# Performance work log

Hardware: AMD Instinct MI355X
Metric: run time of the kernel (lower is better)

## Reference

```python
import jax, jax.numpy as jnp
import numpy as np

EPS = 1e-4  # Moller-Trumbore epsilon from the original

def _dot(a, b):
    return jnp.sum(a * b, axis=-1)

def setup_inputs() -> dict:
    key = jax.random.key(0)
    k1, k2, k3 = jax.random.split(key, 3)
    N, V, F = 2048, 2500, 4096
    p = jax.random.normal(k1, (N, 3), dtype=jnp.float32)
    v = jax.random.normal(k2, (V, 3), dtype=jnp.float32)
    f = jax.random.randint(k3, (F, 3), 0, V, dtype=jnp.int64)
    return {"p": p, "v": v, "f": f}

def reference(p, v, f):
    N = p.shape[0]
    faces = v[f]                      # (F,3,3)
    a, b, c = faces[:, 0], faces[:, 1], faces[:, 2]   # (F,3) each
    pe = p[None]                      # (1,N,3), broadcasts against (F,1,3)

    # --- point-to-triangle distance = min over the 3 edge segments (matches original output math) ---
    e1 = a - b                        # faces[:,0]-faces[:,1]
    e2 = c - b
    e3 = c - a

    def seg(e, ref_pt, q0, q1):
        # s = ((ref_pt - p) . e) / |e|^2, clamped; closest = s*q0 + (1-s)*q1  (original formula kept verbatim)
        m2 = _dot(e, e)[:, None]                       # (F,1)
        s = jnp.clip(_dot(ref_pt[:, None] - pe, e[:, None]) / m2, 0.0, 1.0)[..., None]  # (F,N,1)
        cl = s * q0[:, None] + (1.0 - s) * q1[:, None]  # (F,N,3)
        d = jnp.linalg.norm(cl - pe, axis=-1)           # (F,N)
        return d, cl

    d12, c12 = seg(e1, a, b, a)   # s12 from (p0-p).e1; closest = s*p1+(1-s)*p0
    d23, c23 = seg(e2, c, b, c)   # s23 from (p2-p).e2; closest = s*p1+(1-s)*p2
    d31, c31 = seg(e3, c, a, c)   # s31 from (p2-p).e3; closest = s*p0+(1-s)*p2

    d_all = jnp.stack([d12, d23, d31], axis=0)          # (3,F,N)
    c_all = jnp.stack([c12, c23, c31], axis=0)          # (3,F,N,3)
    which = jnp.argmin(d_all, axis=0)                   # (F,N)
    dist = jnp.min(d_all, axis=0)                       # (F,N)
    closest = jnp.take_along_axis(c_all, which[None, ..., None], axis=0)[0]  # (F,N,3)

    # nearest face per query point
    fidx = jnp.argmin(jnp.abs(dist), axis=0)            # (N,)
    dmin = jnp.take_along_axis(dist, fidx[None], axis=0)  # (1,N)
    closest_p = closest[fidx, jnp.arange(N)]            # (N,3)

    # --- Moller-Trumbore ray-triangle parity test toward mesh centroid ---
    dirv = v.mean(axis=0)[None] - p                     # (N,3)
    me1 = b - a                                         # faces[:,1]-faces[:,0]
    me2 = c - a
    pvec = jnp.cross(dirv[None], me2[:, None])          # (F,N,3)
    det = _dot(me1[:, None], pvec)                      # (F,N)
    tvec = pe - a[:, None]                              # (F,N,3)
    u = _dot(tvec, pvec) / det
    qvec = jnp.cross(tvec, me1[:, None])                # (F,N,3)
    dd = _dot(dirv[None], qvec) / det
    t = _dot(me2[:, None], qvec) / det
    hit = (jnp.abs(det) > EPS) & (u >= 0) & (u <= 1) & (dd >= 0) & (u + dd <= 1) & (t > EPS)
    counts = jnp.sum(hit, axis=0)                       # (N,)
    inside = (0.5 - (counts % 2 == 1).astype(dmin.dtype)) * 2.0  # +1 outside, -1 inside

    dmin = dmin * inside[None]                          # (1,N)
    return (dmin, closest_p)
```

## Files before the change

kernel.cpp:

```cpp
#include <hip/hip_runtime.h>
#include <math.h>

#define TRI_EPS 1e-4f

__global__ __launch_bounds__(256) void prep_kernel(
    const float* __restrict__ v, const int* __restrict__ f,
    float4* __restrict__ fdat, float* __restrict__ vm,
    unsigned long long* __restrict__ keys, int* __restrict__ hcnt,
    int V, int F, int N) {
    const int t = threadIdx.x;
    const int j = blockIdx.x * 256 + t;
    if (j < N) {
        keys[j] = 0xFFFFFFFFFFFFFFFFull;
        hcnt[j] = 0;
    }
    if (j < F) {
        const int i0 = f[3 * j + 0];
        const int i1 = f[3 * j + 1];
        const int i2 = f[3 * j + 2];
        const float ax = v[3 * i0 + 0], ay = v[3 * i0 + 1], az = v[3 * i0 + 2];
        const float bx = v[3 * i1 + 0], by = v[3 * i1 + 1], bz = v[3 * i1 + 2];
        const float cx = v[3 * i2 + 0], cy = v[3 * i2 + 1], cz = v[3 * i2 + 2];
        const float e1x = ax - bx, e1y = ay - by, e1z = az - bz;
        const float e2x = cx - bx, e2y = cy - by, e2z = cz - bz;
        const float e3x = cx - ax, e3y = cy - ay, e3z = cz - az;
        const float m1 = e1x * e1x + e1y * e1y + e1z * e1z;
        const float m2 = e2x * e2x + e2y * e2y + e2z * e2z;
        const float m3 = e3x * e3x + e3y * e3y + e3z * e3z;
        fdat[6 * j + 0] = make_float4(ax, ay, az, 1.f / m1);
        fdat[6 * j + 1] = make_float4(bx, by, bz, 1.f / m2);
        fdat[6 * j + 2] = make_float4(cx, cy, cz, 1.f / m3);
        fdat[6 * j + 3] = make_float4(e1x, e1y, e1z, 0.f);
        fdat[6 * j + 4] = make_float4(e2x, e2y, e2z, 0.f);
        fdat[6 * j + 5] = make_float4(e3x, e3y, e3z, 0.f);
    }
    if (blockIdx.x == 0) {
        __shared__ float sx[256], sy[256], sz[256];
        float x = 0.f, y = 0.f, z = 0.f;
        for (int i = t; i < V; i += 256) {
            x += v[3 * i + 0];
            y += v[3 * i + 1];
            z += v[3 * i + 2];
        }
        sx[t] = x; sy[t] = y; sz[t] = z;
        __syncthreads();
        for (int off = 128; off > 0; off >>= 1) {
            if (t < off) {
                sx[t] += sx[t + off];
                sy[t] += sy[t + off];
                sz[t] += sz[t + off];
            }
            __syncthreads();
        }
        if (t == 0) {
            vm[0] = sx[0] / (float)V;
            vm[1] = sy[0] / (float)V;
            vm[2] = sz[0] / (float)V;
        }
    }
}

struct FP {
    float d1, d2, d3;
    float x1, y1, z1, x2, y2, z2, x3, y3, z3;
    float apx, apy, apz;
};

__device__ __forceinline__ FP face_point(
    const float4 ra, const float4 rb, const float4 rc,
    const float e1x, const float e1y, const float e1z,
    const float e2x, const float e2y, const float e2z,
    const float e3x, const float e3y, const float e3z,
    const float px, const float py, const float pz) {
    FP r;
    const float ax = ra.x, ay = ra.y, az = ra.z;
    const float bx = rb.x, by = rb.y, bz = rb.z;
    const float cx = rc.x, cy = rc.y, cz = rc.z;
    r.apx = ax - px; r.apy = ay - py; r.apz = az - pz;
    const float cpx = cx - px, cpy = cy - py, cpz = cz - pz;

    float s1 = (r.apx * e1x + r.apy * e1y + r.apz * e1z) * ra.w;
    s1 = fminf(fmaxf(s1, 0.f), 1.f);
    const float o1 = 1.f - s1;
    r.x1 = s1 * bx + o1 * ax;
    r.y1 = s1 * by + o1 * ay;
    r.z1 = s1 * bz + o1 * az;
    float ux = r.x1 - px, uy = r.y1 - py, uz = r.z1 - pz;
    r.d1 = ux * ux + uy * uy + uz * uz;

    float s2 = (cpx * e2x + cpy * e2y + cpz * e2z) * rb.w;
    s2 = fminf(fmaxf(s2, 0.f), 1.f);
    const float o2 = 1.f - s2;
    r.x2 = s2 * bx + o2 * cx;
    r.y2 = s2 * by + o2 * cy;
    r.z2 = s2 * bz + o2 * cz;
    ux = r.x2 - px; uy = r.y2 - py; uz = r.z2 - pz;
    r.d2 = ux * ux + uy * uy + uz * uz;

    float s3 = (cpx * e3x + cpy * e3y + cpz * e3z) * rc.w;
    s3 = fminf(fmaxf(s3, 0.f), 1.f);
    const float o3 = 1.f - s3;
    r.x3 = s3 * ax + o3 * cx;
    r.y3 = s3 * ay + o3 * cy;
    r.z3 = s3 * az + o3 * cz;
    ux = r.x3 - px; uy = r.y3 - py; uz = r.z3 - pz;
    r.d3 = ux * ux + uy * uy + uz * uz;
    return r;
}

__device__ __forceinline__ void pair_update(
    const float4 ra, const float4 rb, const float4 rc,
    const float e1x, const float e1y, const float e1z,
    const float e2x, const float e2y, const float e2z,
    const float e3x, const float e3y, const float e3z,
    const float px, const float py, const float pz,
    const float dx, const float dy, const float dz, const int j,
    float& bd2, int& bid, int& hits) {
    const FP r = face_point(ra, rb, rc, e1x, e1y, e1z, e2x, e2y, e2z,
                            e3x, e3y, e3z, px, py, pz);
    float fd2 = r.d1; int eid = 0;
    if (r.d2 < fd2) { fd2 = r.d2; eid = 1; }
    if (r.d3 < fd2) { fd2 = r.d3; eid = 2; }
    if (fd2 < bd2) { bd2 = fd2; bid = (j << 2) | eid; }

    const float pvx = dy * e3z - dz * e3y;
    const float pvy = dz * e3x - dx * e3z;
    const float pvz = dx * e3y - dy * e3x;
    const float det = -(e1x * pvx + e1y * pvy + e1z * pvz);
    const float tu = -(r.apx * pvx + r.apy * pvy + r.apz * pvz);
    const float qvx = r.apy * e1z - r.apz * e1y;
    const float qvy = r.apz * e1x - r.apx * e1z;
    const float qvz = r.apx * e1y - r.apy * e1x;
    const float td = dx * qvx + dy * qvy + dz * qvz;
    const float tn = e3x * qvx + e3y * qvy + e3z * qvz;
    const float adet = fabsf(det);
    const float sd = (det > 0.f) ? 1.f : -1.f;
    const float su = tu * sd;
    const float sq = td * sd;
    const float st = tn * sd;
    if (adet > TRI_EPS && su >= 0.f && su <= adet && sq >= 0.f &&
        (su + sq) <= adet && st > TRI_EPS * adet)
        hits++;
}

__global__ __launch_bounds__(256) void sdf_main(
    const float* __restrict__ p, const float4* __restrict__ fd,
    const float* __restrict__ vm,
    unsigned long long* __restrict__ keys, int* __restrict__ hcnt,
    int N, int F, int C, int CS) {
    const int k = blockIdx.x % C;
    const int pg = blockIdx.x / C;
    const int i = pg * 256 + threadIdx.x;
    if (i >= N) return;

    const float px = p[3 * i + 0];
    const float py = p[3 * i + 1];
    const float pz = p[3 * i + 2];
    const float dx = vm[0] - px;
    const float dy = vm[1] - py;
    const float dz = vm[2] - pz;

    float bd2 = INFINITY;
    int bid = 0x7fffffff;
    int hits = 0;

    const int j0 = k * CS;
    const int j1 = min(F, j0 + CS);
    #pragma unroll 4
    for (int j = j0; j < j1; ++j) {
        const float4 ra  = fd[6 * j + 0];
        const float4 rb  = fd[6 * j + 1];
        const float4 rc  = fd[6 * j + 2];
        const float4 re1 = fd[6 * j + 3];
        const float4 re2 = fd[6 * j + 4];
        const float4 re3 = fd[6 * j + 5];
        pair_update(ra, rb, rc, re1.x, re1.y, re1.z, re2.x, re2.y, re2.z,
                    re3.x, re3.y, re3.z, px, py, pz, dx, dy, dz, j,
                    bd2, bid, hits);
    }
    const unsigned long long key =
        ((unsigned long long)__float_as_uint(bd2) << 32) | (unsigned int)bid;
    atomicMin(&keys[i], key);
    if (hits) atomicAdd(&hcnt[i], hits);
}

__global__ __launch_bounds__(256) void sdf_epilogue(
    const float* __restrict__ p, const float4* __restrict__ fd,
    const unsigned long long* __restrict__ keys, const int* __restrict__ hcnt,
    float* __restrict__ out, int N) {
    const int i = blockIdx.x * 256 + threadIdx.x;
    if (i >= N) return;
    const unsigned long long key = keys[i];
    const float bd2 = __uint_as_float((unsigned int)(key >> 32));
    const int bid = (int)(unsigned int)(key & 0xFFFFFFFFull);
    const int jw = bid >> 2;
    const int eid = bid & 3;
    const float px = p[3 * i + 0];
    const float py = p[3 * i + 1];
    const float pz = p[3 * i + 2];
    const float4 wa  = fd[6 * jw + 0];
    const float4 wb  = fd[6 * jw + 1];
    const float4 wc  = fd[6 * jw + 2];
    const float4 we1 = fd[6 * jw + 3];
    const float4 we2 = fd[6 * jw + 4];
    const float4 we3 = fd[6 * jw + 5];
    const FP r = face_point(wa, wb, wc, we1.x, we1.y, we1.z,
                            we2.x, we2.y, we2.z, we3.x, we3.y, we3.z,
                            px, py, pz);
    float clx = r.x1, cly = r.y1, clz = r.z1;
    if (eid == 1) { clx = r.x2; cly = r.y2; clz = r.z2; }
    if (eid == 2) { clx = r.x3; cly = r.y3; clz = r.z3; }
    const float d = sqrtf(bd2);
    out[i] = (hcnt[i] & 1) ? -d : d;
    out[N + 3 * i + 0] = clx;
    out[N + 3 * i + 1] = cly;
    out[N + 3 * i + 2] = clz;
}

extern "C" void kernel_launch(void* const* d_in, const int* in_sizes, int n_in,
                              void* d_out, int out_size, void* d_ws,
                              size_t ws_size, hipStream_t stream) {
    const float* p = (const float*)d_in[0];
    const float* v = (const float*)d_in[1];
    const int* f = (const int*)d_in[2];
    float* out = (float*)d_out;

    const int N = in_sizes[0] / 3;
    const int V = in_sizes[1] / 3;
    const int F = in_sizes[2] / 3;

    char* base = (char*)d_ws;
    float* vm = (float*)base;
    unsigned long long* keys = (unsigned long long*)(base + 16);
    int* hcnt = (int*)(base + 16 + 8ull * N);
    size_t off = 16 + 12ull * N;
    off = (off + 15) & ~15ull;
    float4* fdat = (float4*)(base + off);

    const int C = 256;
    const int CS = (F + C - 1) / C;
    const int npg = (N + 255) / 256;

    const int gprep = (max(F, N) + 255) / 256;
    prep_kernel<<<gprep, 256, 0, stream>>>(v, f, fdat, vm, keys, hcnt, V, F, N);
    sdf_main<<<npg * C, 256, 0, stream>>>(p, fdat, vm, keys, hcnt, N, F, C, CS);
    sdf_epilogue<<<(N + 255) / 256, 256, 0, stream>>>(p, fdat, keys, hcnt, out, N);
}
```

Baseline: 44.67 us.

## Stage face chunk in shared memory and process two points per thread

Adds a templated main kernel for the case F == 256*16 that loads each block's 16-face chunk (96 float4) into LDS once. Each thread then handles two query points, so every face record read is reused twice and the grid is halved. The intent is to cut global/L1 traffic for face data and to amortise the loads and atomics. In exchange each thread uses more registers, and the fast path is specialised to one exact face count, with a generic fallback kernel for other sizes.

```diff
diff --git a/kernel.cpp b/kernel.cpp
--- a/kernel.cpp
+++ b/kernel.cpp
@@ -143,7 +143,69 @@
         hits++;
 }
 
-__global__ __launch_bounds__(256) void sdf_main(
+template <int CS>
+__global__ __launch_bounds__(256) void sdf_main_t(
+    const float* __restrict__ p, const float4* __restrict__ fd,
+    const float* __restrict__ vm,
+    unsigned long long* __restrict__ keys, int* __restrict__ hcnt,
+    int N, int C) {
+    __shared__ float4 sfd[6 * CS];
+    const int t = threadIdx.x;
+    const int k = blockIdx.x % C;
+    const int pg = blockIdx.x / C;
+    const int j0 = k * CS;
+
+    if (t < 6 * CS) sfd[t] = fd[6 * j0 + t];
+
+    const int i0 = pg * 512 + t;
+    const int i1 = i0 + 256;
+    const bool vA = (i0 < N);
+    const bool vB = (i1 < N);
+    const int lA = vA ? i0 : 0;
+    const int lB = vB ? i1 : 0;
+    const float pAx = p[3 * lA + 0], pAy = p[3 * lA + 1], pAz = p[3 * lA + 2];
+    const float pBx = p[3 * lB + 0], pBy = p[3 * lB + 1], pBz = p[3 * lB + 2];
+    const float vmx = vm[0], vmy = vm[1], vmz = vm[2];
+    const float dAx = vmx - pAx, dAy = vmy - pAy, dAz = vmz - pAz;
+    const float dBx = vmx - pBx, dBy = vmy - pBy, dBz = vmz - pBz;
+
+    float Ad2 = INFINITY; int Aid = 0x7fffffff; int Ah = 0;
+    float Bd2 = INFINITY; int Bid = 0x7fffffff; int Bh = 0;
+
+    __syncthreads();
+
+    #pragma unroll 4
+    for (int jj = 0; jj < CS; ++jj) {
+        const float4 ra  = sfd[6 * jj + 0];
+        const float4 rb  = sfd[6 * jj + 1];
+        const float4 rc  = sfd[6 * jj + 2];
+        const float4 re1 = sfd[6 * jj + 3];
+        const float4 re2 = sfd[6 * jj + 4];
+        const float4 re3 = sfd[6 * jj + 5];
+        const int j = j0 + jj;
+        pair_update(ra, rb, rc, re1.x, re1.y, re1.z, re2.x, re2.y, re2.z,
+                    re3.x, re3.y, re3.z, pAx, pAy, pAz, dAx, dAy, dAz, j,
+                    Ad2, Aid, Ah);
+        pair_update(ra, rb, rc, re1.x, re1.y, re1.z, re2.x, re2.y, re2.z,
+                    re3.x, re3.y, re3.z, pBx, pBy, pBz, dBx, dBy, dBz, j,
+                    Bd2, Bid, Bh);
+    }
+
+    if (vA) {
+        const unsigned long long keyA =
+            ((unsigned long long)__float_as_uint(Ad2) << 32) | (unsigned int)Aid;
+        atomicMin(&keys[i0], keyA);
+        if (Ah) atomicAdd(&hcnt[i0], Ah);
+    }
+    if (vB) {
+        const unsigned long long keyB =
+            ((unsigned long long)__float_as_uint(Bd2) << 32) | (unsigned int)Bid;
+        atomicMin(&keys[i1], keyB);
+        if (Bh) atomicAdd(&hcnt[i1], Bh);
+    }
+}
+
+__global__ __launch_bounds__(256) void sdf_main_g(
     const float* __restrict__ p, const float4* __restrict__ fd,
     const float* __restrict__ vm,
     unsigned long long* __restrict__ keys, int* __restrict__ hcnt,
@@ -152,21 +214,15 @@
     const int pg = blockIdx.x / C;
     const int i = pg * 256 + threadIdx.x;
     if (i >= N) return;
-
     const float px = p[3 * i + 0];
     const float py = p[3 * i + 1];
     const float pz = p[3 * i + 2];
     const float dx = vm[0] - px;
     const float dy = vm[1] - py;
     const float dz = vm[2] - pz;
-
-    float bd2 = INFINITY;
-    int bid = 0x7fffffff;
-    int hits = 0;
-
+    float bd2 = INFINITY; int bid = 0x7fffffff; int hits = 0;
     const int j0 = k * CS;
     const int j1 = min(F, j0 + CS);
-    #pragma unroll 4
     for (int j = j0; j < j1; ++j) {
         const float4 ra  = fd[6 * j + 0];
         const float4 rb  = fd[6 * j + 1];
@@ -238,11 +294,19 @@
     float4* fdat = (float4*)(base + off);
 
     const int C = 256;
-    const int CS = (F + C - 1) / C;
-    const int npg = (N + 255) / 256;
-
     const int gprep = (max(F, N) + 255) / 256;
     prep_kernel<<<gprep, 256, 0, stream>>>(v, f, fdat, vm, keys, hcnt, V, F, N);
-    sdf_main<<<npg * C, 256, 0, stream>>>(p, fdat, vm, keys, hcnt, N, F, C, CS);
-    sdf_epilogue<<<(N + 255) / 256, 256, 0, stream>>>(p, fdat, keys, hcnt, out, N);
-}
+
+    if (F == C * 16) {
+        const int npg = (N + 511) / 512;
+        sdf_main_t<16><<<npg * C, 256, 0, stream>>>(p, fdat, vm, keys, hcnt,
+                                                    N, C);
+    } else {
+        const int CS = (F + C - 1) / C;
+        const int npg = (N + 255) / 256;
+        sdf_main_g<<<npg * C, 256, 0, stream>>>(p, fdat, vm, keys, hcnt,
+                                                N, F, C, CS);
+    }
+    sdf_epilogue<<<(N + 255) / 256, 256, 0, stream>>>(p, fdat, keys, hcnt,
+                                                      out, N);
+}
```

Result: slower. 51.77 us (+15.9%).

## Stage compact face data in LDS and compute distances from edge residuals

Applied to the files above, without the earlier changes.

Adds a compact 5-float4-per-face layout and a templated main kernel that loads each block's 16-face chunk into shared memory once, then loops over it with a compile-time trip count. The per-pair math is rewritten to compute segment residuals directly from edge vectors, without building closest-point coordinates, which cuts arithmetic and register use. A generic fallback kernel covers other face counts. The cost is a second face array written in prep, a block-wide barrier, and an occupancy hint in launch bounds.

```diff
diff --git a/kernel.cpp b/kernel.cpp
--- a/kernel.cpp
+++ b/kernel.cpp
@@ -5,7 +5,8 @@
 
 __global__ __launch_bounds__(256) void prep_kernel(
     const float* __restrict__ v, const int* __restrict__ f,
-    float4* __restrict__ fdat, float* __restrict__ vm,
+    float4* __restrict__ fdat6, float4* __restrict__ fdat5,
+    float* __restrict__ vm,
     unsigned long long* __restrict__ keys, int* __restrict__ hcnt,
     int V, int F, int N) {
     const int t = threadIdx.x;
@@ -27,12 +28,18 @@
         const float m1 = e1x * e1x + e1y * e1y + e1z * e1z;
         const float m2 = e2x * e2x + e2y * e2y + e2z * e2z;
         const float m3 = e3x * e3x + e3y * e3y + e3z * e3z;
-        fdat[6 * j + 0] = make_float4(ax, ay, az, 1.f / m1);
-        fdat[6 * j + 1] = make_float4(bx, by, bz, 1.f / m2);
-        fdat[6 * j + 2] = make_float4(cx, cy, cz, 1.f / m3);
-        fdat[6 * j + 3] = make_float4(e1x, e1y, e1z, 0.f);
-        fdat[6 * j + 4] = make_float4(e2x, e2y, e2z, 0.f);
-        fdat[6 * j + 5] = make_float4(e3x, e3y, e3z, 0.f);
+        const float inv1 = 1.f / m1, inv2 = 1.f / m2, inv3 = 1.f / m3;
+        fdat6[6 * j + 0] = make_float4(ax, ay, az, inv1);
+        fdat6[6 * j + 1] = make_float4(bx, by, bz, inv2);
+        fdat6[6 * j + 2] = make_float4(cx, cy, cz, inv3);
+        fdat6[6 * j + 3] = make_float4(e1x, e1y, e1z, 0.f);
+        fdat6[6 * j + 4] = make_float4(e2x, e2y, e2z, 0.f);
+        fdat6[6 * j + 5] = make_float4(e3x, e3y, e3z, 0.f);
+        fdat5[5 * j + 0] = make_float4(ax, ay, az, inv1);
+        fdat5[5 * j + 1] = make_float4(cx, cy, cz, inv2);
+        fdat5[5 * j + 2] = make_float4(e1x, e1y, e1z, inv3);
+        fdat5[5 * j + 3] = make_float4(e2x, e2y, e2z, 0.f);
+        fdat5[5 * j + 4] = make_float4(e3x, e3y, e3z, 0.f);
     }
     if (blockIdx.x == 0) {
         __shared__ float sx[256], sy[256], sz[256];
@@ -108,29 +115,52 @@
     return r;
 }
 
-__device__ __forceinline__ void pair_update(
-    const float4 ra, const float4 rb, const float4 rc,
-    const float e1x, const float e1y, const float e1z,
-    const float e2x, const float e2y, const float e2z,
-    const float e3x, const float e3y, const float e3z,
+__device__ __forceinline__ void pair_lean(
+    const float4 r0, const float4 r1, const float4 r2,
+    const float4 r3, const float4 r4,
     const float px, const float py, const float pz,
     const float dx, const float dy, const float dz, const int j,
     float& bd2, int& bid, int& hits) {
-    const FP r = face_point(ra, rb, rc, e1x, e1y, e1z, e2x, e2y, e2z,
-                            e3x, e3y, e3z, px, py, pz);
-    float fd2 = r.d1; int eid = 0;
-    if (r.d2 < fd2) { fd2 = r.d2; eid = 1; }
-    if (r.d3 < fd2) { fd2 = r.d3; eid = 2; }
+    const float apx = r0.x - px, apy = r0.y - py, apz = r0.z - pz;
+    const float cpx = r1.x - px, cpy = r1.y - py, cpz = r1.z - pz;
+    const float e1x = r2.x, e1y = r2.y, e1z = r2.z;
+    const float e2x = r3.x, e2y = r3.y, e2z = r3.z;
+    const float e3x = r4.x, e3y = r4.y, e3z = r4.z;
+
+    float s1 = (apx * e1x + apy * e1y + apz * e1z) * r0.w;
+    s1 = fminf(fmaxf(s1, 0.f), 1.f);
+    const float u1x = apx - s1 * e1x;
+    const float u1y = apy - s1 * e1y;
+    const float u1z = apz - s1 * e1z;
+    const float d1 = u1x * u1x + u1y * u1y + u1z * u1z;
+
+    float s2 = (cpx * e2x + cpy * e2y + cpz * e2z) * r1.w;
+    s2 = fminf(fmaxf(s2, 0.f), 1.f);
+    const float u2x = cpx - s2 * e2x;
+    const float u2y = cpy - s2 * e2y;
+    const float u2z = cpz - s2 * e2z;
+    const float d2 = u2x * u2x + u2y * u2y + u2z * u2z;
+
+    float s3 = (cpx * e3x + cpy * e3y + cpz * e3z) * r2.w;
+    s3 = fminf(fmaxf(s3, 0.f), 1.f);
+    const float u3x = cpx - s3 * e3x;
+    const float u3y = cpy - s3 * e3y;
+    const float u3z = cpz - s3 * e3z;
+    const float d3 = u3x * u3x + u3y * u3y + u3z * u3z;
+
+    float fd2 = d1; int eid = 0;
+    if (d2 < fd2) { fd2 = d2; eid = 1; }
+    if (d3 < fd2) { fd2 = d3; eid = 2; }
     if (fd2 < bd2) { bd2 = fd2; bid = (j << 2) | eid; }
 
     const float pvx = dy * e3z - dz * e3y;
     const float pvy = dz * e3x - dx * e3z;
     const float pvz = dx * e3y - dy * e3x;
     const float det = -(e1x * pvx + e1y * pvy + e1z * pvz);
-    const float tu = -(r.apx * pvx + r.apy * pvy + r.apz * pvz);
-    const float qvx = r.apy * e1z - r.apz * e1y;
-    const float qvy = r.apz * e1x - r.apx * e1z;
-    const float qvz = r.apx * e1y - r.apy * e1x;
+    const float tu = -(apx * pvx + apy * pvy + apz * pvz);
+    const float qvx = apy * e1z - apz * e1y;
+    const float qvy = apz * e1x - apx * e1z;
+    const float qvz = apx * e1y - apy * e1x;
     const float td = dx * qvx + dy * qvy + dz * qvz;
     const float tn = e3x * qvx + e3y * qvy + e3z * qvz;
     const float adet = fabsf(det);
@@ -143,8 +173,51 @@
         hits++;
 }
 
-__global__ __launch_bounds__(256) void sdf_main(
-    const float* __restrict__ p, const float4* __restrict__ fd,
+template <int CS>
+__global__ __launch_bounds__(256, 8) void sdf_main_t(
+    const float* __restrict__ p, const float4* __restrict__ fd5,
+    const float* __restrict__ vm,
+    unsigned long long* __restrict__ keys, int* __restrict__ hcnt,
+    int N, int C) {
+    __shared__ float4 sfd[5 * CS];
+    const int t = threadIdx.x;
+    const int k = blockIdx.x % C;
+    const int pg = blockIdx.x / C;
+    const int j0 = k * CS;
+
+    if (t < 5 * CS) sfd[t] = fd5[5 * j0 + t];
+
+    const int i = pg * 256 + t;
+    const bool vld = (i < N);
+    const int li = vld ? i : 0;
+    const float px = p[3 * li + 0];
+    const float py = p[3 * li + 1];
+    const float pz = p[3 * li + 2];
+    const float dx = vm[0] - px;
+    const float dy = vm[1] - py;
+    const float dz = vm[2] - pz;
+
+    float bd2 = INFINITY; int bid = 0x7fffffff; int hits = 0;
+
+    __syncthreads();
+
+    #pragma unroll 2
+    for (int jj = 0; jj < CS; ++jj) {
+        pair_lean(sfd[5 * jj + 0], sfd[5 * jj + 1], sfd[5 * jj + 2],
+                  sfd[5 * jj + 3], sfd[5 * jj + 4],
+                  px, py, pz, dx, dy, dz, j0 + jj, bd2, bid, hits);
+    }
+
+    if (vld) {
+        const unsigned long long key =
+            ((unsigned long long)__float_as_uint(bd2) << 32) | (unsigned int)bid;
+        atomicMin(&keys[i], key);
+        if (hits) atomicAdd(&hcnt[i], hits);
+    }
+}
+
+__global__ __launch_bounds__(256) void sdf_main_g(
+    const float* __restrict__ p, const float4* __restrict__ fd5,
     const float* __restrict__ vm,
     unsigned long long* __restrict__ keys, int* __restrict__ hcnt,
     int N, int F, int C, int CS) {
@@ -152,31 +225,19 @@
     const int pg = blockIdx.x / C;
     const int i = pg * 256 + threadIdx.x;
     if (i >= N) return;
-
     const float px = p[3 * i + 0];
     const float py = p[3 * i + 1];
     const float pz = p[3 * i + 2];
     const float dx = vm[0] - px;
     const float dy = vm[1] - py;
     const float dz = vm[2] - pz;
-
-    float bd2 = INFINITY;
-    int bid = 0x7fffffff;
-    int hits = 0;
-
+    float bd2 = INFINITY; int bid = 0x7fffffff; int hits = 0;
     const int j0 = k * CS;
     const int j1 = min(F, j0 + CS);
-    #pragma unroll 4
     for (int j = j0; j < j1; ++j) {
-        const float4 ra  = fd[6 * j + 0];
-        const float4 rb  = fd[6 * j + 1];
-        const float4 rc  = fd[6 * j + 2];
-        const float4 re1 = fd[6 * j + 3];
-        const float4 re2 = fd[6 * j + 4];
-        const float4 re3 = fd[6 * j + 5];
-        pair_update(ra, rb, rc, re1.x, re1.y, re1.z, re2.x, re2.y, re2.z,
-                    re3.x, re3.y, re3.z, px, py, pz, dx, dy, dz, j,
-                    bd2, bid, hits);
+        pair_lean(fd5[5 * j + 0], fd5[5 * j + 1], fd5[5 * j + 2],
+                  fd5[5 * j + 3], fd5[5 * j + 4],
+                  px, py, pz, dx, dy, dz, j, bd2, bid, hits);
     }
     const unsigned long long key =
         ((unsigned long long)__float_as_uint(bd2) << 32) | (unsigned int)bid;
@@ -185,7 +246,7 @@
 }
 
 __global__ __launch_bounds__(256) void sdf_epilogue(
-    const float* __restrict__ p, const float4* __restrict__ fd,
+    const float* __restrict__ p, const float4* __restrict__ fd6,
     const unsigned long long* __restrict__ keys, const int* __restrict__ hcnt,
     float* __restrict__ out, int N) {
     const int i = blockIdx.x * 256 + threadIdx.x;
@@ -198,12 +259,12 @@
     const float px = p[3 * i + 0];
     const float py = p[3 * i + 1];
     const float pz = p[3 * i + 2];
-    const float4 wa  = fd[6 * jw + 0];
-    const float4 wb  = fd[6 * jw + 1];
-    const float4 wc  = fd[6 * jw + 2];
-    const float4 we1 = fd[6 * jw + 3];
-    const float4 we2 = fd[6 * jw + 4];
-    const float4 we3 = fd[6 * jw + 5];
+    const float4 wa  = fd6[6 * jw + 0];
+    const float4 wb  = fd6[6 * jw + 1];
+    const float4 wc  = fd6[6 * jw + 2];
+    const float4 we1 = fd6[6 * jw + 3];
+    const float4 we2 = fd6[6 * jw + 4];
+    const float4 we3 = fd6[6 * jw + 5];
     const FP r = face_point(wa, wb, wc, we1.x, we1.y, we1.z,
                             we2.x, we2.y, we2.z, we3.x, we3.y, we3.z,
                             px, py, pz);
@@ -235,14 +296,23 @@
     int* hcnt = (int*)(base + 16 + 8ull * N);
     size_t off = 16 + 12ull * N;
     off = (off + 15) & ~15ull;
-    float4* fdat = (float4*)(base + off);
+    float4* fdat6 = (float4*)(base + off);
+    float4* fdat5 = (float4*)(base + off + 6ull * F * sizeof(float4));
 
     const int C = 256;
-    const int CS = (F + C - 1) / C;
+    const int gprep = (max(F, N) + 255) / 256;
+    prep_kernel<<<gprep, 256, 0, stream>>>(v, f, fdat6, fdat5, vm, keys, hcnt,
+                                           V, F, N);
+
     const int npg = (N + 255) / 256;
-
-    const int gprep = (max(F, N) + 255) / 256;
-    prep_kernel<<<gprep, 256, 0, stream>>>(v, f, fdat, vm, keys, hcnt, V, F, N);
-    sdf_main<<<npg * C, 256, 0, stream>>>(p, fdat, vm, keys, hcnt, N, F, C, CS);
-    sdf_epilogue<<<(N + 255) / 256, 256, 0, stream>>>(p, fdat, keys, hcnt, out, N);
-}
+    if (F == C * 16) {
+        sdf_main_t<16><<<npg * C, 256, 0, stream>>>(p, fdat5, vm, keys, hcnt,
+                                                    N, C);
+    } else {
+        const int CS = (F + C - 1) / C;
+        sdf_main_g<<<npg * C, 256, 0, stream>>>(p, fdat5, vm, keys, hcnt,
+                                                N, F, C, CS);
+    }
+    sdf_epilogue<<<(N + 255) / 256, 256, 0, stream>>>(p, fdat6, keys, hcnt,
+                                                      out, N);
+}
```

After: 83.15 us. +86.2%, slower.
